# Optimization experiments

Measured on AMD Instinct MI355X. Metric: run time of the kernel, lower is better.

Reference implementation:

```python
import jax, jax.numpy as jnp
import numpy as np

N = 100000
E = 1600000
NFEAT = 256
NHID = 128


def setup_inputs() -> dict:
    key = jax.random.key(0)
    k1, k2, k3, k4 = jax.random.split(key, 4)
    x = jax.random.normal(k1, (N, NFEAT), dtype=jnp.float32)
    edge_index = jax.random.randint(k2, (2, E), 0, N, dtype=jnp.int64)
    # GCNConv linear weight (stored as [nfeat, nhid] so h = x @ W) + bias
    W = jax.random.normal(k3, (NFEAT, NHID), dtype=jnp.float32) / np.sqrt(NFEAT)
    b = jnp.zeros((NHID,), dtype=jnp.float32)
    # PReLU single shared slope parameter (torch default init 0.25)
    prelu_a = jnp.asarray(0.25, dtype=jnp.float32)
    return {"x": x, "edge_index": edge_index, "W": W, "b": b, "prelu_a": prelu_a}


def _gcn_prelu(x, edge_index, W, b, prelu_a):
    n = x.shape[0]
    # spectral_norm reparametrization: divide weight by its largest singular value
    sigma = jnp.linalg.norm(W.astype(jnp.float32), ord=2)
    h = x @ (W / sigma)  # [N, nhid]
    # add self-loops (PyG GCNConv default)
    loop = jnp.arange(n, dtype=edge_index.dtype)
    row = jnp.concatenate([edge_index[0], loop])  # source
    col = jnp.concatenate([edge_index[1], loop])  # destination
    # symmetric degree normalization: deg from destination counts
    deg = jax.ops.segment_sum(jnp.ones_like(col, dtype=h.dtype), col, num_segments=n)
    dinv = jnp.where(deg > 0, jax.lax.rsqrt(deg), 0.0)
    norm = dinv[row] * dinv[col]  # [E+N]
    msgs = h[row] * norm[:, None]  # [E+N, nhid] gather
    out = jax.ops.segment_sum(msgs, col, num_segments=n) + b  # scatter-add
    # PReLU with shared slope
    return jnp.where(out > 0, out, prelu_a * out)


def reference(x, edge_index, W, b, prelu_a):
    return _gcn_prelu(x, edge_index, W, b, prelu_a)
```

## Files before the change

kernel.cpp:

```cpp
#include <hip/hip_runtime.h>

#define NN 100000
#define EE 1600000
#define NF 256
#define NH 128

#define BK 98
#define BNODE 1024
#define CHUNK 4096
#define NCHUNK ((EE + CHUNK - 1) / CHUNK)
#define CAP 24576

typedef unsigned int u32;
typedef unsigned short u16;
typedef __attribute__((ext_vector_type(8))) short short8;
typedef __attribute__((ext_vector_type(4))) float f32x4;

static __device__ __forceinline__ u16 f2bf(float f) {
  u32 u = __float_as_uint(f);
  u32 r = (u + 0x7FFFu + ((u >> 16) & 1u)) >> 16;
  return (u16)r;
}
static __device__ __forceinline__ float bflo(u32 u) { return __uint_as_float(u << 16); }
static __device__ __forceinline__ float bfhi(u32 u) { return __uint_as_float(u & 0xFFFF0000u); }

__global__ __launch_bounds__(256) void k_spec(const float* __restrict__ W,
                                              u16* __restrict__ Wt2,
                                              float* __restrict__ sig) {
  __shared__ __align__(16) char MB[65536];
  __shared__ float diag[128];
  __shared__ float red[256];
  __shared__ float uvec[128];
  __shared__ float itrS;
  __shared__ int jmS;
  int t = threadIdx.x;
  int l = t & 63, w = t >> 6;
  int p = l & 15, q = l >> 4;

  for (int base = t * 4; base < NF * NH; base += 256 * 4) {
    float4 v = *(const float4*)&W[base];
    int k = base >> 7, c0 = base & 127;
#pragma unroll
    for (int i = 0; i < 4; i++) {
      int c = c0 + i;
      int inner = (k * 2) ^ ((c & 7) << 4);
      *(u16*)(MB + c * 512 + inner) = f2bf(((const float*)&v)[i]);
    }
  }
  __syncthreads();
  for (int u = t; u < 16384; u += 256) {
    int h = u * 2;
    int n = h >> 12;
    int rem = h & 4095;
    int ks = rem >> 9;
    int rem2 = rem & 511;
    int ll = rem2 >> 3;
    int j = rem2 & 7;
    int c = n * 16 + (ll & 15);
    int k = ks * 32 + ((ll >> 4) << 3) + j;
    ((u32*)Wt2)[u] = *(u32*)(MB + c * 512 + ((2 * k) ^ ((c & 7) << 4)));
  }

  f32x4 acc[2][8] = {};
#pragma unroll
  for (int ks = 0; ks < 8; ks++) {
    int kb = (ks * 32 + q * 8) * 2;
    short8 afr[2], bfr[8];
#pragma unroll
    for (int m = 0; m < 2; m++) {
      int ra = w * 32 + m * 16 + p;
      afr[m] = *(const short8*)(MB + ra * 512 + (kb ^ ((ra & 7) << 4)));
    }
#pragma unroll
    for (int n = 0; n < 8; n++) {
      int r = n * 16 + p;
      bfr[n] = *(const short8*)(MB + r * 512 + (kb ^ ((r & 7) << 4)));
    }
#pragma unroll
    for (int m = 0; m < 2; m++)
#pragma unroll
      for (int n = 0; n < 8; n++)
        acc[m][n] = __builtin_amdgcn_mfma_f32_16x16x32_bf16(afr[m], bfr[n], acc[m][n], 0, 0, 0);
  }
#pragma unroll
  for (int m = 0; m < 2; m++)
#pragma unroll
    for (int n = 0; n < 8; n++)
#pragma unroll
      for (int g = 0; g < 4; g++) {
        int r = w * 32 + m * 16 + q * 4 + g;
        int c = n * 16 + p;
        if (r == c) diag[r] = acc[m][n][g];
      }
  __syncthreads();
  if (t == 0) {
    float s = 0.f;
    for (int i = 0; i < 128; i++) s += diag[i];
    itrS = 1.0f / s;
  }
  __syncthreads();
  {
    float itr = itrS;
    char* mb0 = MB;
#pragma unroll
    for (int m = 0; m < 2; m++)
#pragma unroll
      for (int n = 0; n < 8; n++)
#pragma unroll
        for (int g = 0; g < 4; g++) {
          int r = w * 32 + m * 16 + q * 4 + g;
          int c = n * 16 + p;
          *(u16*)(mb0 + r * 256 + ((c * 2) ^ ((r & 7) << 4))) = f2bf(acc[m][n][g] * itr);
        }
  }

  char* src = MB;
  char* dst = MB + 32768;
  for (int s = 0; s < 8; s++) {
    __syncthreads();
    f32x4 mac[2][8] = {};
#pragma unroll
    for (int ks = 0; ks < 4; ks++) {
      int kb = (ks * 32 + q * 8) * 2;
      short8 afr[2], bfr[8];
#pragma unroll
      for (int m = 0; m < 2; m++) {
        int ra = w * 32 + m * 16 + p;
        afr[m] = *(const short8*)(src + ra * 256 + (kb ^ ((ra & 7) << 4)));
      }
#pragma unroll
      for (int n = 0; n < 8; n++) {
        int r = n * 16 + p;
        bfr[n] = *(const short8*)(src + r * 256 + (kb ^ ((r & 7) << 4)));
      }
#pragma unroll
      for (int m = 0; m < 2; m++)
#pragma unroll
        for (int n = 0; n < 8; n++)
          mac[m][n] = __builtin_amdgcn_mfma_f32_16x16x32_bf16(afr[m], bfr[n], mac[m][n], 0, 0, 0);
    }
#pragma unroll
    for (int m = 0; m < 2; m++)
#pragma unroll
      for (int n = 0; n < 8; n++)
#pragma unroll
        for (int g = 0; g < 4; g++) {
          int r = w * 32 + m * 16 + q * 4 + g;
          int c = n * 16 + p;
          if (r == c) diag[r] = mac[m][n][g];
        }
    __syncthreads();
    if (t == 0) {
      float ss = 0.f;
      for (int i = 0; i < 128; i++) ss += diag[i];
      itrS = 1.0f / ss;
    }
    __syncthreads();
    float it2 = itrS;
#pragma unroll
    for (int m = 0; m < 2; m++)
#pragma unroll
      for (int n = 0; n < 8; n++)
#pragma unroll
        for (int g = 0; g < 4; g++) {
          int r = w * 32 + m * 16 + q * 4 + g;
          int c = n * 16 + p;
          *(u16*)(dst + r * 256 + ((c * 2) ^ ((r & 7) << 4))) = f2bf(mac[m][n][g] * it2);
        }
    char* tmp = src; src = dst; dst = tmp;
  }
  __syncthreads();

  if (t == 0) {
    int jm = 0;
    float bm = diag[0];
    for (int i = 1; i < 128; i++)
      if (diag[i] > bm) { bm = diag[i]; jm = i; }
    jmS = jm;
  }
  __syncthreads();
  int jm = jmS;
  if (t < 128) {
    u16 hv = *(u16*)(src + jm * 256 + ((t * 2) ^ ((jm & 7) << 4)));
    uvec[t] = __uint_as_float(((u32)hv) << 16);
  }
  __syncthreads();
  {
    float a2 = 0.f;
    const float* wr = &W[t * NH];
    for (int k = 0; k < NH; k++) a2 += wr[k] * uvec[k];
    red[t] = a2 * a2;
  }
  __syncthreads();
  if (t == 0) {
    float num = 0.f;
    for (int i = 0; i < 256; i++) num += red[i];
    float den = 0.f;
    for (int i = 0; i < 128; i++) den += uvec[i] * uvec[i];
    sig[0] = rsqrtf(num / den);
  }
}

__global__ __launch_bounds__(256) void k_p1(const int* __restrict__ row,
                                            const int* __restrict__ col,
                                            u32* __restrict__ gcur,
                                            u32* __restrict__ binned) {
  __shared__ u32 keybuf[CHUNK];
  __shared__ unsigned char bktbuf[CHUNK];
  __shared__ u32 hist[BK], lstart[BK], lofs[BK], gb[BK];
  int t = threadIdx.x;
  if (t < BK) hist[t] = 0;
  __syncthreads();
  int e0 = blockIdx.x * CHUNK;
  int n = min(CHUNK, EE - e0);
  for (int i = t; i < n; i += 256) {
    u32 d = (u32)col[e0 + i];
    atomicAdd(&hist[d >> 10], 1u);
  }
  __syncthreads();
  if (t == 0) {
    u32 s = 0;
    for (int b = 0; b < BK; b++) { lstart[b] = s; lofs[b] = s; s += hist[b]; }
  }
  __syncthreads();
  if (t < BK && hist[t]) gb[t] = (u32)t * CAP + atomicAdd(&gcur[t], hist[t]);
  __syncthreads();
  for (int i = t; i < n; i += 256) {
    u32 d = (u32)col[e0 + i];
    u32 s = (u32)row[e0 + i];
    u32 b = d >> 10;
    u32 p = atomicAdd(&lofs[b], 1u);
    keybuf[p] = ((d & 1023u) << 17) | s;
    bktbuf[p] = (unsigned char)b;
  }
  __syncthreads();
  for (int i = t; i < n; i += 256) {
    u32 b = bktbuf[i];
    binned[gb[b] + ((u32)i - lstart[b])] = keybuf[i];
  }
}

__global__ __launch_bounds__(1024) void k_p2(const u32* __restrict__ binned,
                                             const u32* __restrict__ gcur,
                                             uint2* __restrict__ offdeg,
                                             float* __restrict__ dinv,
                                             int* __restrict__ csr) {
  __shared__ u32 hist[BNODE];
  __shared__ u32 loff[BNODE];
  __shared__ u32 cur[BNODE];
  __shared__ u32 stage[CAP];
  int b = blockIdx.x, t = threadIdx.x;
  u32 base = (u32)b * CAP;
  u32 cnt = gcur[b];
  hist[t] = 0;
  __syncthreads();
  for (u32 i = t; i < cnt; i += BNODE) {
    u32 key = binned[base + i];
    atomicAdd(&hist[key >> 17], 1u);
  }
  __syncthreads();
  u32 v = hist[t];
  loff[t] = v;
  __syncthreads();
  for (int d = 1; d < BNODE; d <<= 1) {
    u32 x = loff[t];
    u32 y = (t >= d) ? loff[t - d] : 0u;
    __syncthreads();
    loff[t] = x + y;
    __syncthreads();
  }
  u32 ex = loff[t] - v;
  cur[t] = ex;
  int g = b * BNODE + t;
  if (g < NN) {
    offdeg[g] = make_uint2(base + ex, base + ex + v);
    dinv[g] = rsqrtf((float)(v + 1u));
  }
  __syncthreads();
  if (cnt <= CAP) {
    for (u32 i = t; i < cnt; i += BNODE) {
      u32 key = binned[base + i];
      u32 p = atomicAdd(&cur[key >> 17], 1u);
      stage[p] = key & 0x1FFFFu;
    }
    __syncthreads();
    for (u32 i = t; i < cnt; i += BNODE) csr[base + i] = (int)stage[i];
  } else {
    for (u32 i = t; i < cnt; i += BNODE) {
      u32 key = binned[base + i];
      u32 p = atomicAdd(&cur[key >> 17], 1u);
      csr[base + p] = (int)(key & 0x1FFFFu);
    }
  }
}

__global__ __launch_bounds__(256) void k_mfma(const float* __restrict__ x,
                                              const u16* __restrict__ Wt2,
                                              const float* __restrict__ dinv,
                                              u16* __restrict__ hs) {
  __shared__ __align__(16) char LB[65536];
  int t = threadIdx.x;
  int l = t & 63, w = t >> 6;
  int row0 = blockIdx.x * 128;
  int lr = l & 15;
  int lk = (l >> 4) * 8;

  const float4* x4 = (const float4*)x;
#pragma unroll 4
  for (int i = t; i < 128 * 64; i += 256) {
    int r = i >> 6;
    int cq = i & 63;
    int gr = row0 + r;
    if (gr >= NN) gr = NN - 1;
    float4 v = x4[(size_t)gr * 64 + cq];
    uint2 wv;
    wv.x = (u32)f2bf(v.x) | ((u32)f2bf(v.y) << 16);
    wv.y = (u32)f2bf(v.z) | ((u32)f2bf(v.w) << 16);
    int kb = cq * 8;
    *(uint2*)(LB + r * 512 + (kb ^ ((r & 7) << 4))) = wv;
  }
  __syncthreads();

  int rbase = w * 32;
  f32x4 acc[2][8] = {};
#pragma unroll
  for (int ks = 0; ks < 8; ks++) {
    short8 bfr[8];
#pragma unroll
    for (int n = 0; n < 8; n++)
      bfr[n] = *(const short8*)&Wt2[(size_t)(((n * 8 + ks) * 64) + l) * 8];
    short8 afr[2];
#pragma unroll
    for (int m = 0; m < 2; m++) {
      int r = rbase + m * 16 + lr;
      int kb = (ks * 32 + lk) * 2;
      afr[m] = *(const short8*)(LB + r * 512 + (kb ^ ((r & 7) << 4)));
    }
#pragma unroll
    for (int m = 0; m < 2; m++)
#pragma unroll
      for (int n = 0; n < 8; n++)
        acc[m][n] = __builtin_amdgcn_mfma_f32_16x16x32_bf16(afr[m], bfr[n], acc[m][n], 0, 0, 0);
  }

  __syncthreads();
  u16* tile = (u16*)LB;
#pragma unroll
  for (int m = 0; m < 2; m++) {
    int rbl = w * 32 + m * 16 + (l >> 4) * 4;
    float dv[4];
#pragma unroll
    for (int g = 0; g < 4; g++) {
      int r = row0 + rbl + g;
      dv[g] = (r < NN) ? dinv[r] : 0.f;
    }
#pragma unroll
    for (int n = 0; n < 8; n++)
#pragma unroll
      for (int g = 0; g < 4; g++)
        tile[(rbl + g) * 128 + n * 16 + lr] = f2bf(acc[m][n][g] * dv[g]);
  }
  __syncthreads();
  const uint4* tl = (const uint4*)tile;
  size_t outb = (size_t)row0 * NH;
#pragma unroll
  for (int k = 0; k < 8; k++) {
    int u = t + k * 256;
    if (row0 + (u >> 4) < NN) *(uint4*)&hs[outb + (size_t)u * 8] = tl[u];
  }
}

__global__ __launch_bounds__(256) void k_gather(const u16* __restrict__ hs,
                                                const int* __restrict__ csr,
                                                const uint2* __restrict__ offdeg,
                                                const float* __restrict__ dinv,
                                                const float* __restrict__ b,
                                                const float* __restrict__ pa,
                                                const float* __restrict__ sig,
                                                float* __restrict__ out) {
  int wid = threadIdx.x >> 6;
  int lane = threadIdx.x & 63;
  int n = blockIdx.x * 4 + wid;
  if (n >= NN) return;
  uint2 od = offdeg[n];
  u32 s0 = od.x, s1 = od.y;
  const u32* hrow = (const u32*)hs;
  float ax, ay;
  {
    u32 u = hrow[(size_t)n * 64 + lane];
    ax = bflo(u); ay = bfhi(u);
  }
  u32 e = s0;
  for (; e + 8 <= s1; e += 8) {
    int i0 = csr[e],     i1 = csr[e + 1], i2 = csr[e + 2], i3 = csr[e + 3];
    int i4 = csr[e + 4], i5 = csr[e + 5], i6 = csr[e + 6], i7 = csr[e + 7];
    u32 u0 = hrow[(size_t)i0 * 64 + lane];
    u32 u1 = hrow[(size_t)i1 * 64 + lane];
    u32 u2 = hrow[(size_t)i2 * 64 + lane];
    u32 u3 = hrow[(size_t)i3 * 64 + lane];
    u32 u4 = hrow[(size_t)i4 * 64 + lane];
    u32 u5 = hrow[(size_t)i5 * 64 + lane];
    u32 u6 = hrow[(size_t)i6 * 64 + lane];
    u32 u7 = hrow[(size_t)i7 * 64 + lane];
    ax += bflo(u0) + bflo(u1) + bflo(u2) + bflo(u3)
        + bflo(u4) + bflo(u5) + bflo(u6) + bflo(u7);
    ay += bfhi(u0) + bfhi(u1) + bfhi(u2) + bfhi(u3)
        + bfhi(u4) + bfhi(u5) + bfhi(u6) + bfhi(u7);
  }
  for (; e + 4 <= s1; e += 4) {
    int i0 = csr[e], i1 = csr[e + 1], i2 = csr[e + 2], i3 = csr[e + 3];
    u32 u0 = hrow[(size_t)i0 * 64 + lane];
    u32 u1 = hrow[(size_t)i1 * 64 + lane];
    u32 u2 = hrow[(size_t)i2 * 64 + lane];
    u32 u3 = hrow[(size_t)i3 * 64 + lane];
    ax += bflo(u0) + bflo(u1) + bflo(u2) + bflo(u3);
    ay += bfhi(u0) + bfhi(u1) + bfhi(u2) + bfhi(u3);
  }
  for (; e < s1; e++) {
    u32 u = hrow[(size_t)csr[e] * 64 + lane];
    ax += bflo(u); ay += bfhi(u);
  }
  float dv = dinv[n] * sig[0];
  float2 bb = *(const float2*)&b[lane * 2];
  float a = pa[0];
  float v0 = ax * dv + bb.x;
  float v1 = ay * dv + bb.y;
  float2 o;
  o.x = v0 > 0.f ? v0 : a * v0;
  o.y = v1 > 0.f ? v1 : a * v1;
  *(float2*)&out[(size_t)n * NH + lane * 2] = o;
}

extern "C" void kernel_launch(void* const* d_in, const int* in_sizes, int n_in,
                              void* d_out, int out_size, void* d_ws, size_t ws_size,
                              hipStream_t stream) {
  const float* x = (const float*)d_in[0];
  const int* ei = (const int*)d_in[1];
  const float* W = (const float*)d_in[2];
  const float* b = (const float*)d_in[3];
  const float* pa = (const float*)d_in[4];
  float* out = (float*)d_out;
  const int* row = ei;
  const int* col = ei + EE;

  char* base = (char*)d_ws;
  size_t o = 0;
  auto alloc = [&](size_t bytes) -> void* {
    void* p = base + o;
    o += (bytes + 63) & ~(size_t)63;
    return p;
  };
  u32* gcur = (u32*)alloc(BK * 4);
  float* sig = (float*)alloc(64);
  float* dinv = (float*)alloc((size_t)NN * 4);
  uint2* offdeg = (uint2*)alloc((size_t)NN * 8);
  u32* binned = (u32*)alloc((size_t)BK * CAP * 4);
  int* csr = (int*)alloc((size_t)BK * CAP * 4);
  u16* Wt2 = (u16*)alloc((size_t)NF * NH * 2);
  u16* hs = (u16*)alloc((size_t)NN * NH * 2);
  (void)ws_size; (void)in_sizes; (void)n_in; (void)out_size;

  hipMemsetAsync(gcur, 0, BK * 4, stream);
  k_spec<<<1, 256, 0, stream>>>(W, Wt2, sig);
  k_p1<<<NCHUNK, 256, 0, stream>>>(row, col, gcur, binned);
  k_p2<<<BK, BNODE, 0, stream>>>(binned, gcur, offdeg, dinv, csr);
  k_mfma<<<(NN + 127) / 128, 256, 0, stream>>>(x, Wt2, dinv, hs);
  k_gather<<<(NN + 3) / 4, 256, 0, stream>>>(hs, csr, offdeg, dinv, b, pa, sig, out);
}
```

Baseline: 186.9 us.

## Merge spectral-norm kernel into edge binning launch and parallelize its reductions

The single-block spectral-norm kernel is folded into the edge-binning kernel as one extra block, so the serial power-iteration work runs alongside the binning blocks instead of as its own launch. The serial thread-0 loops for trace sums, argmax and the final norm are replaced with shared-memory tree reductions. The x-load loop unroll in the MFMA kernel is also raised. In exchange, every binning block now reserves the larger 68 KB shared allocation, which may lower the number of binning blocks resident per CU.

```diff
diff --git a/kernel.cpp b/kernel.cpp
--- a/kernel.cpp
+++ b/kernel.cpp
@@ -24,20 +24,66 @@
 static __device__ __forceinline__ float bflo(u32 u) { return __uint_as_float(u << 16); }
 static __device__ __forceinline__ float bfhi(u32 u) { return __uint_as_float(u & 0xFFFF0000u); }
 
-__global__ __launch_bounds__(256) void k_spec(const float* __restrict__ W,
-                                              u16* __restrict__ Wt2,
-                                              float* __restrict__ sig) {
-  __shared__ __align__(16) char MB[65536];
-  __shared__ float diag[128];
-  __shared__ float red[256];
-  __shared__ float uvec[128];
-  __shared__ float itrS;
-  __shared__ int jmS;
+__global__ __launch_bounds__(256) void k_p1s(const int* __restrict__ row,
+                                             const int* __restrict__ col,
+                                             u32* __restrict__ gcur,
+                                             u32* __restrict__ binned,
+                                             const float* __restrict__ W,
+                                             u16* __restrict__ Wt2,
+                                             float* __restrict__ sig) {
+  __shared__ __align__(16) char SM[69632];
   int t = threadIdx.x;
+
+  if (blockIdx.x < NCHUNK) {
+    u32* keybuf = (u32*)SM;
+    unsigned char* bktbuf = (unsigned char*)(SM + 16384);
+    u32* hist = (u32*)(SM + 20480);
+    u32* lstart = (u32*)(SM + 20992);
+    u32* lofs = (u32*)(SM + 21504);
+    u32* gb = (u32*)(SM + 22016);
+    if (t < BK) hist[t] = 0;
+    __syncthreads();
+    int e0 = blockIdx.x * CHUNK;
+    int n = min(CHUNK, EE - e0);
+    for (int i = t; i < n; i += 256) {
+      u32 d = (u32)col[e0 + i];
+      atomicAdd(&hist[d >> 10], 1u);
+    }
+    __syncthreads();
+    if (t == 0) {
+      u32 s = 0;
+      for (int b = 0; b < BK; b++) { lstart[b] = s; lofs[b] = s; s += hist[b]; }
+    }
+    __syncthreads();
+    if (t < BK && hist[t]) gb[t] = (u32)t * CAP + atomicAdd(&gcur[t], hist[t]);
+    __syncthreads();
+    for (int i = t; i < n; i += 256) {
+      u32 d = (u32)col[e0 + i];
+      u32 s = (u32)row[e0 + i];
+      u32 b = d >> 10;
+      u32 p = atomicAdd(&lofs[b], 1u);
+      keybuf[p] = ((d & 1023u) << 17) | s;
+      bktbuf[p] = (unsigned char)b;
+    }
+    __syncthreads();
+    for (int i = t; i < n; i += 256) {
+      u32 b = bktbuf[i];
+      binned[gb[b] + ((u32)i - lstart[b])] = keybuf[i];
+    }
+    return;
+  }
+
+  char* MB = SM;
+  float* diag = (float*)(SM + 65536);
+  float* red = (float*)(SM + 66048);
+  float* uvec = (float*)(SM + 67072);
+  int* jdx = (int*)(SM + 67584);
+  float* itrS = (float*)(SM + 68096);
+  int* jmS = (int*)(SM + 68100);
   int l = t & 63, w = t >> 6;
   int p = l & 15, q = l >> 4;
 
-  for (int base = t * 4; base < NF * NH; base += 256 * 4) {
+  for (int base = t * 4; base < NF * NH; base += 1024) {
     float4 v = *(const float4*)&W[base];
     int k = base >> 7, c0 = base & 127;
 #pragma unroll
@@ -93,15 +139,13 @@
         if (r == c) diag[r] = acc[m][n][g];
       }
   __syncthreads();
-  if (t == 0) {
-    float s = 0.f;
-    for (int i = 0; i < 128; i++) s += diag[i];
-    itrS = 1.0f / s;
-  }
+  if (t < 128) red[t] = diag[t];
+  __syncthreads();
+  for (int d = 64; d > 0; d >>= 1) { if (t < d) red[t] += red[t + d]; __syncthreads(); }
+  if (t == 0) itrS[0] = 1.0f / red[0];
   __syncthreads();
   {
-    float itr = itrS;
-    char* mb0 = MB;
+    float itr = itrS[0];
 #pragma unroll
     for (int m = 0; m < 2; m++)
 #pragma unroll
@@ -110,7 +154,7 @@
         for (int g = 0; g < 4; g++) {
           int r = w * 32 + m * 16 + q * 4 + g;
           int c = n * 16 + p;
-          *(u16*)(mb0 + r * 256 + ((c * 2) ^ ((r & 7) << 4))) = f2bf(acc[m][n][g] * itr);
+          *(u16*)(MB + r * 256 + ((c * 2) ^ ((r & 7) << 4))) = f2bf(acc[m][n][g] * itr);
         }
   }
 
@@ -150,13 +194,12 @@
           if (r == c) diag[r] = mac[m][n][g];
         }
     __syncthreads();
-    if (t == 0) {
-      float ss = 0.f;
-      for (int i = 0; i < 128; i++) ss += diag[i];
-      itrS = 1.0f / ss;
-    }
-    __syncthreads();
-    float it2 = itrS;
+    if (t < 128) red[t] = diag[t];
+    __syncthreads();
+    for (int d = 64; d > 0; d >>= 1) { if (t < d) red[t] += red[t + d]; __syncthreads(); }
+    if (t == 0) itrS[0] = 1.0f / red[0];
+    __syncthreads();
+    float it2 = itrS[0];
 #pragma unroll
     for (int m = 0; m < 2; m++)
 #pragma unroll
@@ -171,15 +214,15 @@
   }
   __syncthreads();
 
-  if (t == 0) {
-    int jm = 0;
-    float bm = diag[0];
-    for (int i = 1; i < 128; i++)
-      if (diag[i] > bm) { bm = diag[i]; jm = i; }
-    jmS = jm;
-  }
-  __syncthreads();
-  int jm = jmS;
+  if (t < 128) { red[t] = diag[t]; jdx[t] = t; }
+  __syncthreads();
+  for (int d = 64; d > 0; d >>= 1) {
+    if (t < d && red[t + d] > red[t]) { red[t] = red[t + d]; jdx[t] = jdx[t + d]; }
+    __syncthreads();
+  }
+  if (t == 0) jmS[0] = jdx[0];
+  __syncthreads();
+  int jm = jmS[0];
   if (t < 128) {
     u16 hv = *(u16*)(src + jm * 256 + ((t * 2) ^ ((jm & 7) << 4)));
     uvec[t] = __uint_as_float(((u32)hv) << 16);
@@ -192,52 +235,14 @@
     red[t] = a2 * a2;
   }
   __syncthreads();
-  if (t == 0) {
-    float num = 0.f;
-    for (int i = 0; i < 256; i++) num += red[i];
-    float den = 0.f;
-    for (int i = 0; i < 128; i++) den += uvec[i] * uvec[i];
-    sig[0] = rsqrtf(num / den);
-  }
-}
-
-__global__ __launch_bounds__(256) void k_p1(const int* __restrict__ row,
-                                            const int* __restrict__ col,
-                                            u32* __restrict__ gcur,
-                                            u32* __restrict__ binned) {
-  __shared__ u32 keybuf[CHUNK];
-  __shared__ unsigned char bktbuf[CHUNK];
-  __shared__ u32 hist[BK], lstart[BK], lofs[BK], gb[BK];
-  int t = threadIdx.x;
-  if (t < BK) hist[t] = 0;
-  __syncthreads();
-  int e0 = blockIdx.x * CHUNK;
-  int n = min(CHUNK, EE - e0);
-  for (int i = t; i < n; i += 256) {
-    u32 d = (u32)col[e0 + i];
-    atomicAdd(&hist[d >> 10], 1u);
-  }
-  __syncthreads();
-  if (t == 0) {
-    u32 s = 0;
-    for (int b = 0; b < BK; b++) { lstart[b] = s; lofs[b] = s; s += hist[b]; }
-  }
-  __syncthreads();
-  if (t < BK && hist[t]) gb[t] = (u32)t * CAP + atomicAdd(&gcur[t], hist[t]);
-  __syncthreads();
-  for (int i = t; i < n; i += 256) {
-    u32 d = (u32)col[e0 + i];
-    u32 s = (u32)row[e0 + i];
-    u32 b = d >> 10;
-    u32 p = atomicAdd(&lofs[b], 1u);
-    keybuf[p] = ((d & 1023u) << 17) | s;
-    bktbuf[p] = (unsigned char)b;
-  }
-  __syncthreads();
-  for (int i = t; i < n; i += 256) {
-    u32 b = bktbuf[i];
-    binned[gb[b] + ((u32)i - lstart[b])] = keybuf[i];
-  }
+  for (int d = 128; d > 0; d >>= 1) { if (t < d) red[t] += red[t + d]; __syncthreads(); }
+  if (t == 0) itrS[0] = red[0];
+  __syncthreads();
+  float num = itrS[0];
+  if (t < 128) red[t] = uvec[t] * uvec[t];
+  __syncthreads();
+  for (int d = 64; d > 0; d >>= 1) { if (t < d) red[t] += red[t + d]; __syncthreads(); }
+  if (t == 0) sig[0] = rsqrtf(num / red[0]);
 }
 
 __global__ __launch_bounds__(1024) void k_p2(const u32* __restrict__ binned,
@@ -306,7 +311,7 @@
   int lk = (l >> 4) * 8;
 
   const float4* x4 = (const float4*)x;
-#pragma unroll 4
+#pragma unroll 8
   for (int i = t; i < 128 * 64; i += 256) {
     int r = i >> 6;
     int cq = i & 63;
@@ -461,8 +466,7 @@
   (void)ws_size; (void)in_sizes; (void)n_in; (void)out_size;
 
   hipMemsetAsync(gcur, 0, BK * 4, stream);
-  k_spec<<<1, 256, 0, stream>>>(W, Wt2, sig);
-  k_p1<<<NCHUNK, 256, 0, stream>>>(row, col, gcur, binned);
+  k_p1s<<<NCHUNK + 1, 256, 0, stream>>>(row, col, gcur, binned, W, Wt2, sig);
   k_p2<<<BK, BNODE, 0, stream>>>(binned, gcur, offdeg, dinv, csr);
   k_mfma<<<(NN + 127) / 128, 256, 0, stream>>>(x, Wt2, dinv, hs);
   k_gather<<<(NN + 3) / 4, 256, 0, stream>>>(hs, csr, offdeg, dinv, b, pa, sig, out);
```

Result: faster. 178.2 us (-4.6%).
